# Kernel tuning notes

Hardware: AMD Instinct MI355X
Metric: run time of the kernel (lower is better)

## Reference

```python
import jax, jax.numpy as jnp
import numpy as np

B, S, D, L = 4, 512, 768, 64


def setup_inputs() -> dict:
    key = jax.random.key(0)
    k1, k2, k3, k4, k5 = jax.random.split(key, 5)
    return {
        "head": jax.random.normal(k1, (B, S, D), dtype=jnp.float32),
        "dep": jax.random.normal(k2, (B, S, D), dtype=jnp.float32),
        "label_U_diag": jax.random.normal(k3, (L, D), dtype=jnp.float32) * 0.02,
        "label_W": jax.random.normal(k4, (L, 2 * D), dtype=jnp.float32) * 0.02,
        "label_b": jax.random.normal(k5, (L,), dtype=jnp.float32) * 0.02,
    }


def reference(head, dep, label_U_diag, label_W, label_b):
    # t1[b,l,i,o] = sum_d head[b,i,d] * U[l,d] * dep[b,o,d]  (diag bilinear)
    t1 = jnp.einsum('bid,ld,bod->blio', head, label_U_diag, dep)
    # Linear term: instead of materializing the O(S^2 * 2D) concat tensor,
    # split W into head/dep halves and broadcast-add two O(S*L) matmuls.
    d = head.shape[-1]
    Wh, Wd = label_W[:, :d], label_W[:, d:]
    t2_h = jnp.einsum('bid,ld->bli', head, Wh)  # [B, L, S] (row / head index)
    t2_d = jnp.einsum('bod,ld->blo', dep, Wd)   # [B, L, S] (col / dep index)
    return t1 + t2_h[:, :, :, None] + t2_d[:, :, None, :] + label_b[None, :, None, None]
```

## Files before the change

kernel.cpp:

```cpp
#include <hip/hip_runtime.h>

typedef __bf16 bf16;
typedef __bf16 bf16x8 __attribute__((ext_vector_type(8)));
typedef float  f32x4  __attribute__((ext_vector_type(4)));

#define S 512
#define DD 768
#define LL 64
#define BB 4

__device__ __forceinline__ void async_copy16(const void* g, void* l) {
    __builtin_amdgcn_global_load_lds(
        (const __attribute__((address_space(1))) unsigned int*)g,
        (__attribute__((address_space(3))) unsigned int*)l,
        16, 0, 0);
}

__device__ __forceinline__ bf16x8 scale_cvt(float4 a, float4 b, float4 ua, float4 ub) {
    bf16x8 p;
    p[0] = (bf16)(a.x * ua.x); p[1] = (bf16)(a.y * ua.y);
    p[2] = (bf16)(a.z * ua.z); p[3] = (bf16)(a.w * ua.w);
    p[4] = (bf16)(b.x * ub.x); p[5] = (bf16)(b.y * ub.y);
    p[6] = (bf16)(b.z * ub.z); p[7] = (bf16)(b.w * ub.w);
    return p;
}

__global__ void cvt_dep_kernel(const float* __restrict__ dep, bf16* __restrict__ out) {
    int idx = (blockIdx.x * 256 + threadIdx.x) * 8;
    float4 a = *(const float4*)(dep + idx);
    float4 c = *(const float4*)(dep + idx + 4);
    bf16x8 p;
    p[0] = (bf16)a.x; p[1] = (bf16)a.y; p[2] = (bf16)a.z; p[3] = (bf16)a.w;
    p[4] = (bf16)c.x; p[5] = (bf16)c.y; p[6] = (bf16)c.z; p[7] = (bf16)c.w;
    *(bf16x8*)(out + idx) = p;
}

__global__ void t2_kernel(const float* __restrict__ head, const float* __restrict__ dep,
                          const float* __restrict__ W, const float* __restrict__ bias,
                          float* __restrict__ t2h, float* __restrict__ t2d) {
    __shared__ float Wl[16][DD];
    __shared__ float red[64][4][16];
    int bid = blockIdx.x;
    int sel = bid >> 7;
    int r   = bid & 127;
    int b   = r >> 5;
    int lg  = (r >> 3) & 3;
    int ic  = r & 7;
    const float* src = sel ? dep : head;
    int t = threadIdx.x;

    for (int l16 = 0; l16 < 16; ++l16) {
        const float* wp = W + (size_t)(lg * 16 + l16) * (2 * DD) + sel * DD;
        Wl[l16][t]       = wp[t];
        Wl[l16][t + 256] = wp[t + 256];
        Wl[l16][t + 512] = wp[t + 512];
    }
    __syncthreads();

    int iq = t >> 2, dq = t & 3;
    int i  = ic * 64 + iq;
    const float* rowp = src + (size_t)(b * S + i) * DD;
    float acc[16];
#pragma unroll
    for (int l16 = 0; l16 < 16; ++l16) acc[l16] = 0.f;
    for (int it = 0; it < 48; ++it) {
        int d = dq * 4 + it * 16;
        float4 x = *(const float4*)(rowp + d);
#pragma unroll
        for (int l16 = 0; l16 < 16; ++l16) {
            float4 wv = *(const float4*)&Wl[l16][d];
            acc[l16] += x.x * wv.x + x.y * wv.y + x.z * wv.z + x.w * wv.w;
        }
    }
#pragma unroll
    for (int l16 = 0; l16 < 16; ++l16) red[iq][dq][l16] = acc[l16];
    __syncthreads();

    int iq2 = t >> 2, l4 = t & 3;
    float* dst = sel ? t2d : t2h;
#pragma unroll
    for (int j = 0; j < 4; ++j) {
        int l16 = l4 * 4 + j;
        float v = red[iq2][0][l16] + red[iq2][1][l16] + red[iq2][2][l16] + red[iq2][3][l16];
        if (sel) v += bias[lg * 16 + l16];
        dst[(size_t)(b * LL + lg * 16 + l16) * S + ic * 64 + iq2] = v;
    }
}

__global__ __launch_bounds__(256, 2) void biaffine_main(
    const float* __restrict__ head, const bf16* __restrict__ depb,
    const float* __restrict__ U, const float* __restrict__ t2h,
    const float* __restrict__ t2d, float* __restrict__ out) {
    __shared__ __align__(16) bf16 As[128][32];
    __shared__ __align__(16) bf16 Bs[128][32];
    __shared__ __align__(16) float Ulds[DD];

    const int tid  = threadIdx.x;
    const int lane = tid & 63;
    const int w    = tid >> 6;
    const int bi0  = (blockIdx.x & 3) << 7;
    const int bo0  = (blockIdx.x >> 2) << 7;
    const int l    = blockIdx.y;
    const int b    = blockIdx.z;

    {
        const float* up = U + (size_t)l * DD;
        Ulds[tid]       = up[tid];
        Ulds[tid + 256] = up[tid + 256];
        Ulds[tid + 512] = up[tid + 512];
    }

    const int r1 = tid >> 2;
    const int cp = tid & 3;
    const int sw = (r1 >> 1) & 3;
    const int ca = cp ^ sw;
    const float* hp0 = head + (size_t)(b * S + bi0 + r1) * DD + ca * 8;
    const float* hp1 = hp0 + (size_t)64 * DD;
    bf16* awr0 = &As[r1][cp * 8];
    bf16* awr1 = &As[r1 + 64][cp * 8];

    const int rB0 = w * 32 + (lane >> 2);
    const int rB1 = rB0 + 16;
    const int cpB = lane & 3;
    const bf16* bp0 = depb + (size_t)(b * S + bo0 + rB0) * DD + (cpB ^ ((rB0 >> 1) & 3)) * 8;
    const bf16* bp1 = depb + (size_t)(b * S + bo0 + rB1) * DD + (cpB ^ ((rB1 >> 1) & 3)) * 8;
    bf16* bw0 = &Bs[w * 32][0];
    bf16* bw1 = &Bs[w * 32 + 16][0];

    const int wr = w & 1, wc = w >> 1;
    const int mrow = lane & 15, q = lane >> 4;
    const bf16* ap[4];
    const bf16* bp[4];
#pragma unroll
    for (int mi = 0; mi < 4; ++mi) {
        int rowA = wr * 64 + mi * 16 + mrow;
        ap[mi] = &As[rowA][(q ^ ((rowA >> 1) & 3)) * 8];
        int rowB = wc * 64 + mi * 16 + mrow;
        bp[mi] = &Bs[rowB][(q ^ ((rowB >> 1) & 3)) * 8];
    }

    f32x4 acc[4][4];
#pragma unroll
    for (int mi = 0; mi < 4; ++mi)
#pragma unroll
        for (int ni = 0; ni < 4; ++ni)
            acc[mi][ni] = (f32x4){0.f, 0.f, 0.f, 0.f};

    __syncthreads();

    const float* h0 = hp0;
    const float* h1 = hp1;
    const bf16*  g0 = bp0;
    const bf16*  g1 = bp1;
    for (int kt = 0; kt < 24; ++kt) {
        float4 h0a = *(const float4*)(h0);
        float4 h0b = *(const float4*)(h0 + 4);
        float4 h1a = *(const float4*)(h1);
        float4 h1b = *(const float4*)(h1 + 4);
        async_copy16(g0, bw0);
        async_copy16(g1, bw1);
        const float* uu = &Ulds[kt * 32 + ca * 8];
        float4 ua = *(const float4*)(uu);
        float4 ub = *(const float4*)(uu + 4);
        *(bf16x8*)awr0 = scale_cvt(h0a, h0b, ua, ub);
        *(bf16x8*)awr1 = scale_cvt(h1a, h1b, ua, ub);
        h0 += 32; h1 += 32; g0 += 32; g1 += 32;
        __syncthreads();

        bf16x8 af[4], bfr[4];
#pragma unroll
        for (int mi = 0; mi < 4; ++mi) af[mi]  = *(const bf16x8*)ap[mi];
#pragma unroll
        for (int ni = 0; ni < 4; ++ni) bfr[ni] = *(const bf16x8*)bp[ni];
#pragma unroll
        for (int mi = 0; mi < 4; ++mi)
#pragma unroll
            for (int ni = 0; ni < 4; ++ni)
                acc[mi][ni] = __builtin_amdgcn_mfma_f32_16x16x32_bf16(af[mi], bfr[ni], acc[mi][ni], 0, 0, 0);
        __syncthreads();
    }

    const size_t bl = (size_t)(b * LL + l);
    const float* t2hp = t2h + bl * S + bi0 + wr * 64;
    const float* t2dp = t2d + bl * S + bo0 + wc * 64;
    float* outbase = out + bl * S * S;
#pragma unroll
    for (int mi = 0; mi < 4; ++mi) {
        float4 th = *(const float4*)&t2hp[mi * 16 + q * 4];
        int row0 = bi0 + wr * 64 + mi * 16 + q * 4;
#pragma unroll
        for (int ni = 0; ni < 4; ++ni) {
            int col = bo0 + wc * 64 + ni * 16 + mrow;
            float td = t2dp[ni * 16 + mrow];
            float* op = outbase + (size_t)row0 * S + col;
            op[0 * S] = acc[mi][ni][0] + th.x + td;
            op[1 * S] = acc[mi][ni][1] + th.y + td;
            op[2 * S] = acc[mi][ni][2] + th.z + td;
            op[3 * S] = acc[mi][ni][3] + th.w + td;
        }
    }
}

extern "C" void kernel_launch(void* const* d_in, const int* in_sizes, int n_in,
                              void* d_out, int out_size, void* d_ws, size_t ws_size,
                              hipStream_t stream) {
    const float* head = (const float*)d_in[0];
    const float* dep  = (const float*)d_in[1];
    const float* U    = (const float*)d_in[2];
    const float* W    = (const float*)d_in[3];
    const float* bias = (const float*)d_in[4];
    float* out = (float*)d_out;

    char*  ws   = (char*)d_ws;
    bf16*  depb = (bf16*)ws;
    float* t2h  = (float*)(ws + 3145728);
    float* t2d  = (float*)(ws + 3145728 + 524288);

    cvt_dep_kernel<<<768, 256, 0, stream>>>(dep, depb);
    t2_kernel<<<256, 256, 0, stream>>>(head, dep, W, bias, t2h, t2d);
    biaffine_main<<<dim3(16, LL, BB), 256, 0, stream>>>(head, depb, U, t2h, t2d, out);
}
```

Baseline: 396.3 us.

## Precompute U-scaled bf16 head per label and stream both operands asynchronously

```diff
diff --git a/kernel.cpp b/kernel.cpp
--- a/kernel.cpp
+++ b/kernel.cpp
@@ -35,36 +35,53 @@
     *(bf16x8*)(out + idx) = p;
 }
 
+__global__ void scaleA_kernel(const float* __restrict__ head, const float* __restrict__ U,
+                              bf16* __restrict__ out) {
+    int l = blockIdx.y;
+    int b = blockIdx.z;
+    int e = blockIdx.x * 2048 + threadIdx.x * 8;
+    int d = e - (e / DD) * DD;
+    const float* hp = head + (size_t)b * S * DD + e;
+    const float* up = U + l * DD + d;
+    float4 a  = *(const float4*)hp;
+    float4 c  = *(const float4*)(hp + 4);
+    float4 ua = *(const float4*)up;
+    float4 ub = *(const float4*)(up + 4);
+    *(bf16x8*)(out + (size_t)(b * LL + l) * S * DD + e) = scale_cvt(a, c, ua, ub);
+}
+
 __global__ void t2_kernel(const float* __restrict__ head, const float* __restrict__ dep,
                           const float* __restrict__ W, const float* __restrict__ bias,
                           float* __restrict__ t2h, float* __restrict__ t2d) {
     __shared__ float Wl[16][DD];
-    __shared__ float red[64][4][16];
+    __shared__ float red[32][8][16];
     int bid = blockIdx.x;
-    int sel = bid >> 7;
-    int r   = bid & 127;
-    int b   = r >> 5;
-    int lg  = (r >> 3) & 3;
-    int ic  = r & 7;
+    int sel = bid >> 8;
+    int r   = bid & 255;
+    int b   = r >> 6;
+    int lg  = (r >> 4) & 3;
+    int ic  = r & 15;
     const float* src = sel ? dep : head;
     int t = threadIdx.x;
 
-    for (int l16 = 0; l16 < 16; ++l16) {
-        const float* wp = W + (size_t)(lg * 16 + l16) * (2 * DD) + sel * DD;
-        Wl[l16][t]       = wp[t];
-        Wl[l16][t + 256] = wp[t + 256];
-        Wl[l16][t + 512] = wp[t + 512];
+#pragma unroll
+    for (int k = 0; k < 12; ++k) {
+        int idx = t + k * 256;
+        int row = idx / 192;
+        int col = idx - row * 192;
+        const float* wp = W + (size_t)(lg * 16 + row) * (2 * DD) + sel * DD + col * 4;
+        *(float4*)&Wl[row][col * 4] = *(const float4*)wp;
     }
     __syncthreads();
 
-    int iq = t >> 2, dq = t & 3;
-    int i  = ic * 64 + iq;
+    int iq = t >> 3, dq = t & 7;
+    int i  = ic * 32 + iq;
     const float* rowp = src + (size_t)(b * S + i) * DD;
     float acc[16];
 #pragma unroll
     for (int l16 = 0; l16 < 16; ++l16) acc[l16] = 0.f;
-    for (int it = 0; it < 48; ++it) {
-        int d = dq * 4 + it * 16;
+    for (int it = 0; it < 24; ++it) {
+        int d = dq * 4 + it * 32;
         float4 x = *(const float4*)(rowp + d);
 #pragma unroll
         for (int l16 = 0; l16 < 16; ++l16) {
@@ -76,24 +93,25 @@
     for (int l16 = 0; l16 < 16; ++l16) red[iq][dq][l16] = acc[l16];
     __syncthreads();
 
-    int iq2 = t >> 2, l4 = t & 3;
+    int iq2 = t >> 3, l2 = t & 7;
     float* dst = sel ? t2d : t2h;
 #pragma unroll
-    for (int j = 0; j < 4; ++j) {
-        int l16 = l4 * 4 + j;
-        float v = red[iq2][0][l16] + red[iq2][1][l16] + red[iq2][2][l16] + red[iq2][3][l16];
+    for (int j = 0; j < 2; ++j) {
+        int l16 = l2 * 2 + j;
+        float v = 0.f;
+#pragma unroll
+        for (int dq2 = 0; dq2 < 8; ++dq2) v += red[iq2][dq2][l16];
         if (sel) v += bias[lg * 16 + l16];
-        dst[(size_t)(b * LL + lg * 16 + l16) * S + ic * 64 + iq2] = v;
+        dst[(size_t)(b * LL + lg * 16 + l16) * S + ic * 32 + iq2] = v;
     }
 }
 
 __global__ __launch_bounds__(256, 2) void biaffine_main(
-    const float* __restrict__ head, const bf16* __restrict__ depb,
-    const float* __restrict__ U, const float* __restrict__ t2h,
-    const float* __restrict__ t2d, float* __restrict__ out) {
+    const bf16* __restrict__ Ah, const bf16* __restrict__ depb,
+    const float* __restrict__ t2h, const float* __restrict__ t2d,
+    float* __restrict__ out) {
     __shared__ __align__(16) bf16 As[128][32];
     __shared__ __align__(16) bf16 Bs[128][32];
-    __shared__ __align__(16) float Ulds[DD];
 
     const int tid  = threadIdx.x;
     const int lane = tid & 63;
@@ -103,29 +121,19 @@
     const int l    = blockIdx.y;
     const int b    = blockIdx.z;
 
-    {
-        const float* up = U + (size_t)l * DD;
-        Ulds[tid]       = up[tid];
-        Ulds[tid + 256] = up[tid + 256];
-        Ulds[tid + 512] = up[tid + 512];
-    }
-
-    const int r1 = tid >> 2;
-    const int cp = tid & 3;
-    const int sw = (r1 >> 1) & 3;
-    const int ca = cp ^ sw;
-    const float* hp0 = head + (size_t)(b * S + bi0 + r1) * DD + ca * 8;
-    const float* hp1 = hp0 + (size_t)64 * DD;
-    bf16* awr0 = &As[r1][cp * 8];
-    bf16* awr1 = &As[r1 + 64][cp * 8];
-
-    const int rB0 = w * 32 + (lane >> 2);
-    const int rB1 = rB0 + 16;
-    const int cpB = lane & 3;
-    const bf16* bp0 = depb + (size_t)(b * S + bo0 + rB0) * DD + (cpB ^ ((rB0 >> 1) & 3)) * 8;
-    const bf16* bp1 = depb + (size_t)(b * S + bo0 + rB1) * DD + (cpB ^ ((rB1 >> 1) & 3)) * 8;
-    bf16* bw0 = &Bs[w * 32][0];
-    bf16* bw1 = &Bs[w * 32 + 16][0];
+    const int rS  = w * 32 + (lane >> 2);
+    const int cpS = lane & 3;
+    const int sw  = (rS >> 1) & 3;
+    const int ca  = cpS ^ sw;
+    const bf16* Abase = Ah + (size_t)(b * LL + l) * S * DD;
+    const bf16* ga0 = Abase + (size_t)(bi0 + rS) * DD + ca * 8;
+    const bf16* ga1 = ga0 + (size_t)16 * DD;
+    const bf16* gb0 = depb + (size_t)(b * S + bo0 + rS) * DD + ca * 8;
+    const bf16* gb1 = gb0 + (size_t)16 * DD;
+    bf16* lwa0 = &As[w * 32][0];
+    bf16* lwa1 = &As[w * 32 + 16][0];
+    bf16* lwb0 = &Bs[w * 32][0];
+    bf16* lwb1 = &Bs[w * 32 + 16][0];
 
     const int wr = w & 1, wc = w >> 1;
     const int mrow = lane & 15, q = lane >> 4;
@@ -146,25 +154,12 @@
         for (int ni = 0; ni < 4; ++ni)
             acc[mi][ni] = (f32x4){0.f, 0.f, 0.f, 0.f};
 
-    __syncthreads();
-
-    const float* h0 = hp0;
-    const float* h1 = hp1;
-    const bf16*  g0 = bp0;
-    const bf16*  g1 = bp1;
     for (int kt = 0; kt < 24; ++kt) {
-        float4 h0a = *(const float4*)(h0);
-        float4 h0b = *(const float4*)(h0 + 4);
-        float4 h1a = *(const float4*)(h1);
-        float4 h1b = *(const float4*)(h1 + 4);
-        async_copy16(g0, bw0);
-        async_copy16(g1, bw1);
-        const float* uu = &Ulds[kt * 32 + ca * 8];
-        float4 ua = *(const float4*)(uu);
-        float4 ub = *(const float4*)(uu + 4);
-        *(bf16x8*)awr0 = scale_cvt(h0a, h0b, ua, ub);
-        *(bf16x8*)awr1 = scale_cvt(h1a, h1b, ua, ub);
-        h0 += 32; h1 += 32; g0 += 32; g1 += 32;
+        async_copy16(ga0, lwa0);
+        async_copy16(ga1, lwa1);
+        async_copy16(gb0, lwb0);
+        async_copy16(gb1, lwb1);
+        ga0 += 32; ga1 += 32; gb0 += 32; gb1 += 32;
         __syncthreads();
 
         bf16x8 af[4], bfr[4];
@@ -212,11 +207,13 @@
     float* out = (float*)d_out;
 
     char*  ws   = (char*)d_ws;
-    bf16*  depb = (bf16*)ws;
-    float* t2h  = (float*)(ws + 3145728);
-    float* t2d  = (float*)(ws + 3145728 + 524288);
+    bf16*  Ahb  = (bf16*)ws;
+    bf16*  depb = (bf16*)(ws + 201326592);
+    float* t2h  = (float*)(ws + 201326592 + 3145728);
+    float* t2d  = (float*)(ws + 201326592 + 3145728 + 524288);
 
     cvt_dep_kernel<<<768, 256, 0, stream>>>(dep, depb);
-    t2_kernel<<<256, 256, 0, stream>>>(head, dep, W, bias, t2h, t2d);
-    biaffine_main<<<dim3(16, LL, BB), 256, 0, stream>>>(head, depb, U, t2h, t2d, out);
-}
+    scaleA_kernel<<<dim3(192, LL, BB), 256, 0, stream>>>(head, U, Ahb);
+    t2_kernel<<<512, 256, 0, stream>>>(head, dep, W, bias, t2h, t2d);
+    biaffine_main<<<dim3(16, LL, BB), 256, 0, stream>>>(Ahb, depb, t2h, t2d, out);
+}
```

Result: slower. 460.5 us (+16.2%).
